# Kernel tuning notes

Measured on AMD Instinct MI355X. Metric: run time of the kernel, lower is better.

## Reference

```python
import jax, jax.numpy as jnp
import numpy as np

N_NODES = 100000
N_EDGES = 1600000
N_GRAPHS = 4096
IN_DIM = 14
HID = 128


def setup_inputs() -> dict:
    key = jax.random.key(0)
    ks = jax.random.split(key, 12)
    x = jax.random.normal(ks[0], (N_NODES, IN_DIM), dtype=jnp.float32)
    edge_index = jax.random.randint(ks[1], (2, N_EDGES), 0, N_NODES, dtype=jnp.int64)
    batch = jnp.sort(jax.random.randint(ks[2], (N_NODES,), 0, N_GRAPHS, dtype=jnp.int64))

    def lin(k, fan_in, fan_out):
        bound = 1.0 / np.sqrt(fan_in)
        kw, kb = jax.random.split(k)
        W = jax.random.uniform(kw, (fan_in, fan_out), minval=-bound, maxval=bound, dtype=jnp.float32)
        b = jax.random.uniform(kb, (fan_out,), minval=-bound, maxval=bound, dtype=jnp.float32)
        return W, b

    W1a, b1a = lin(ks[3], IN_DIM, HID)
    W1b, b1b = lin(ks[4], HID, HID)
    W2a, b2a = lin(ks[5], HID, HID)
    W2b, b2b = lin(ks[6], HID, HID)
    Wout, bout = lin(ks[7], HID, HID)
    return dict(x=x, edge_index=edge_index, batch=batch,
                W1a=W1a, b1a=b1a, W1b=W1b, b1b=b1b,
                W2a=W2a, b2a=b2a, W2b=W2b, b2b=b2b,
                Wout=Wout, bout=bout)


def _gin_conv(x, src, dst, Wa, ba, Wb, bb):
    # aggregate: sum of neighbor features x[src] scattered to dst; eps = 0
    agg = jax.ops.segment_sum(x[src], dst, num_segments=N_NODES)
    h = x + agg  # (1 + eps) * x + sum_j x_j, eps=0
    h = jax.nn.relu(h @ Wa + ba)
    return h @ Wb + bb


def reference(x, edge_index, batch, W1a, b1a, W1b, b1b, W2a, b2a, W2b, b2b, Wout, bout):
    src, dst = edge_index[0], edge_index[1]
    h = jax.nn.relu(_gin_conv(x, src, dst, W1a, b1a, W1b, b1b))
    h = jax.nn.relu(_gin_conv(h, src, dst, W2a, b2a, W2b, b2b))
    # global mean pool over graphs
    sums = jax.ops.segment_sum(h, batch, num_segments=N_GRAPHS)          # [G, HID]
    cnts = jax.ops.segment_sum(jnp.ones((h.shape[0],), h.dtype), batch, num_segments=N_GRAPHS)
    pooled = sums / jnp.maximum(cnts, 1.0)[:, None]
    # dropout is identity in eval mode
    return pooled @ Wout + bout
```

## Files before the change

### kernel.cpp

```cpp
#include <hip/hip_runtime.h>
#include <hip/hip_bf16.h>

#define NODES  100000
#define EDGES  1600000
#define GRAPHS 4096
#define HID    128
#define INDIM  14
#define NPART  8
#define PART_SZ ((NODES + NPART - 1) / NPART)
#define BPG    256
#define CSTRIDE 64
#define LDST   136

typedef float f32x4 __attribute__((ext_vector_type(4)));
typedef short bf16x8 __attribute__((ext_vector_type(8)));

__device__ __forceinline__ unsigned packbf(float a, float b) {
    __hip_bfloat162 t;
    t.x = __float2bfloat16(a);
    t.y = __float2bfloat16(b);
    return *(unsigned*)&t;
}
__device__ __forceinline__ void acc8(float* a, uint4 v) {
    a[0] += __uint_as_float(v.x << 16);
    a[1] += __uint_as_float(v.x & 0xffff0000u);
    a[2] += __uint_as_float(v.y << 16);
    a[3] += __uint_as_float(v.y & 0xffff0000u);
    a[4] += __uint_as_float(v.z << 16);
    a[5] += __uint_as_float(v.z & 0xffff0000u);
    a[6] += __uint_as_float(v.w << 16);
    a[7] += __uint_as_float(v.w & 0xffff0000u);
}


__global__ void k_zero_int(int* __restrict__ p, int n) {
    int i = blockIdx.x * 256 + threadIdx.x;
    if (i < n) p[i] = 0;
}

__global__ __launch_bounds__(256) void k_fill_fx(const int* __restrict__ src,
                                                 const int* __restrict__ dst,
                                                 int* __restrict__ cnt,
                                                 int* __restrict__ csr) {
    const int g = blockIdx.x & (NPART - 1);
    const int blk = blockIdx.x >> 3;
    const int lo = g * PART_SZ;
    for (int e = blk * 256 + threadIdx.x; e < EDGES; e += BPG * 256) {
        int d = __builtin_nontemporal_load(&dst[e]);
        if ((unsigned)(d - lo) < PART_SZ) {
            int s = __builtin_nontemporal_load(&src[e]);
            int pos = atomicAdd(&cnt[d], 1);
            if (pos < CSTRIDE) csr[d * CSTRIDE + pos] = s;
        }
    }
}


__global__ void k_w_cvt4(const float* __restrict__ Wa, const float* __restrict__ Wb,
                         const float* __restrict__ Wc, const float* __restrict__ Wd,
                         __hip_bfloat16* __restrict__ Ta, __hip_bfloat16* __restrict__ Tb,
                         __hip_bfloat16* __restrict__ Tc, __hip_bfloat16* __restrict__ Td) {
    int which = blockIdx.x >> 6;
    int idx = (blockIdx.x & 63) * 256 + threadIdx.x;
    const float* W = which == 0 ? Wa : which == 1 ? Wb : which == 2 ? Wc : Wd;
    __hip_bfloat16* T = which == 0 ? Ta : which == 1 ? Tb : which == 2 ? Tc : Td;
    int n = idx & 127, k = idx >> 7;
    T[n * HID + k] = __float2bfloat16(W[k * HID + n]);
}

template <int RELU, int TO_LDS>
__device__ __forceinline__ void mfma_slice16(const __hip_bfloat16* lds_in,
                                             const __hip_bfloat16* __restrict__ Wt,
                                             const float* __restrict__ bias,
                                             __hip_bfloat16* lds_out,
                                             __hip_bfloat16* __restrict__ gout,
                                             int row0, int tid) {
    const int wave = tid >> 6;
    const int lane = tid & 63;
    const int rl = lane & 15;
    const int kb = lane >> 4;

    bf16x8 afrag[4];
#pragma unroll
    for (int kc = 0; kc < 4; kc++)
        afrag[kc] = *(const bf16x8*)(lds_in + rl * LDST + kc * 32 + kb * 8);

#pragma unroll
    for (int s = 0; s < 2; s++) {
        const int n = wave * 2 + s;
        f32x4 acc = (f32x4){0.f, 0.f, 0.f, 0.f};
        const __hip_bfloat16* Bp = Wt + (size_t)(n * 16 + rl) * HID + kb * 8;
#pragma unroll
        for (int kc = 0; kc < 4; kc++) {
            bf16x8 bfrag = *(const bf16x8*)(Bp + kc * 32);
            acc = __builtin_amdgcn_mfma_f32_16x16x32_bf16(afrag[kc], bfrag, acc, 0, 0, 0);
        }
        const int col = n * 16 + rl;
        const float bv = bias[col];
#pragma unroll
        for (int j = 0; j < 4; j++) {
            int rloc = kb * 4 + j;
            float v = acc[j] + bv;
            if (RELU) v = fmaxf(v, 0.f);
            if (TO_LDS)
                lds_out[rloc * LDST + col] = __float2bfloat16(v);
            else
                gout[(size_t)(row0 + rloc) * HID + col] = __float2bfloat16(v);
        }
    }
}


__global__ __launch_bounds__(256) void k_l1(const float* __restrict__ x,
                                            const int* __restrict__ cnt,
                                            const int* __restrict__ csr,
                                            const float* __restrict__ W1a,
                                            const float* __restrict__ b1a,
                                            const __hip_bfloat16* __restrict__ Wt1b,
                                            const float* __restrict__ b1b,
                                            __hip_bfloat16* __restrict__ h1) {
    __shared__ float p14[16][16];
    __shared__ __hip_bfloat16 t[16 * LDST];
    const int row0 = blockIdx.x * 16;
    const int tid = threadIdx.x;

    {
        int n = tid >> 4, d = tid & 15;
        int node = row0 + n;
        if (d < INDIM) {
            int len = cnt[node];
            if (len > CSTRIDE) len = CSTRIDE;
            const int* cp = csr + (size_t)node * CSTRIDE;
            float acc = x[node * INDIM + d];
            int e = 0;
            for (; e + 3 < len; e += 4) {
                int s0 = cp[e], s1 = cp[e + 1], s2 = cp[e + 2], s3 = cp[e + 3];
                acc += x[s0 * INDIM + d] + x[s1 * INDIM + d] +
                       x[s2 * INDIM + d] + x[s3 * INDIM + d];
            }
            for (; e < len; e++) acc += x[cp[e] * INDIM + d];
            p14[n][d] = acc;
        }
    }
    __syncthreads();

    for (int i = tid; i < 512; i += 256) {
        int r = i >> 5, c4 = (i & 31) << 2;
        float4 bv = *(const float4*)&b1a[c4];
        float ax = bv.x, ay = bv.y, az = bv.z, aw = bv.w;
#pragma unroll
        for (int k = 0; k < INDIM; k++) {
            float a = p14[r][k];
            float4 w = *(const float4*)&W1a[k * HID + c4];
            ax += a * w.x; ay += a * w.y; az += a * w.z; aw += a * w.w;
        }
        unsigned p0 = packbf(fmaxf(ax, 0.f), fmaxf(ay, 0.f));
        unsigned p1 = packbf(fmaxf(az, 0.f), fmaxf(aw, 0.f));
        *(uint2*)&t[r * LDST + c4] = make_uint2(p0, p1);
    }
    __syncthreads();

    mfma_slice16<1, 0>(t, Wt1b, b1b, nullptr, h1, row0, tid);
}


__global__ __launch_bounds__(256) void k_l2(const uint4* __restrict__ H,
                                            const int* __restrict__ cnt,
                                            const int* __restrict__ csr,
                                            const __hip_bfloat16* __restrict__ Wt2a,
                                            const float* __restrict__ b2a,
                                            const __hip_bfloat16* __restrict__ Wt2b,
                                            const float* __restrict__ b2b,
                                            __hip_bfloat16* __restrict__ h2) {
    __shared__ __hip_bfloat16 ta[16 * LDST];
    __shared__ __hip_bfloat16 tb[16 * LDST];
    const int row0 = blockIdx.x * 16;
    const int tid = threadIdx.x;

    {
        int n = tid >> 4, q = tid & 15;
        int node = row0 + n;
        int len = cnt[node];
        if (len > CSTRIDE) len = CSTRIDE;
        const int* cp = csr + (size_t)node * CSTRIDE;
        float a[8];
        uint4 v = H[(size_t)node * 16 + q];
        a[0] = __uint_as_float(v.x << 16);
        a[1] = __uint_as_float(v.x & 0xffff0000u);
        a[2] = __uint_as_float(v.y << 16);
        a[3] = __uint_as_float(v.y & 0xffff0000u);
        a[4] = __uint_as_float(v.z << 16);
        a[5] = __uint_as_float(v.z & 0xffff0000u);
        a[6] = __uint_as_float(v.w << 16);
        a[7] = __uint_as_float(v.w & 0xffff0000u);
        int e = 0;
        for (; e + 3 < len; e += 4) {
            int s0 = cp[e], s1 = cp[e + 1], s2 = cp[e + 2], s3 = cp[e + 3];
            uint4 v0 = H[(size_t)s0 * 16 + q];
            uint4 v1 = H[(size_t)s1 * 16 + q];
            uint4 v2 = H[(size_t)s2 * 16 + q];
            uint4 v3 = H[(size_t)s3 * 16 + q];
            acc8(a, v0); acc8(a, v1); acc8(a, v2); acc8(a, v3);
        }
        for (; e < len; e++) {
            uint4 vv = H[(size_t)cp[e] * 16 + q];
            acc8(a, vv);
        }
        uint4 o;
        o.x = packbf(a[0], a[1]);
        o.y = packbf(a[2], a[3]);
        o.z = packbf(a[4], a[5]);
        o.w = packbf(a[6], a[7]);
        *(uint4*)&ta[n * LDST + q * 8] = o;
    }
    __syncthreads();

    mfma_slice16<1, 1>(ta, Wt2a, b2a, tb, nullptr, row0, tid);
    __syncthreads();

    mfma_slice16<1, 0>(tb, Wt2b, b2b, nullptr, h2, row0, tid);
}


__global__ __launch_bounds__(256) void k_head(const __hip_bfloat16* __restrict__ A,
                                              const __hip_bfloat16* __restrict__ Wt,
                                              const float* __restrict__ bias,
                                              float* __restrict__ out) {
    const int wave = threadIdx.x >> 6;
    const int lane = threadIdx.x & 63;
    const int row0 = blockIdx.x * 64 + wave * 16;
    const int rl = lane & 15;
    const int kb = lane >> 4;

    const __hip_bfloat16* Ap = A + (size_t)(row0 + rl) * HID + kb * 8;
    bf16x8 afrag[4];
#pragma unroll
    for (int kc = 0; kc < 4; kc++) afrag[kc] = *(const bf16x8*)(Ap + kc * 32);

#pragma unroll
    for (int n = 0; n < 8; n++) {
        f32x4 acc = (f32x4){0.f, 0.f, 0.f, 0.f};
        const __hip_bfloat16* Bp = Wt + (size_t)(n * 16 + rl) * HID + kb * 8;
#pragma unroll
        for (int kc = 0; kc < 4; kc++) {
            bf16x8 bfrag = *(const bf16x8*)(Bp + kc * 32);
            acc = __builtin_amdgcn_mfma_f32_16x16x32_bf16(afrag[kc], bfrag, acc, 0, 0, 0);
        }
        const int col = n * 16 + rl;
        const float bv = bias[col];
#pragma unroll
        for (int j = 0; j < 4; j++)
            out[(size_t)(row0 + kb * 4 + j) * HID + col] = acc[j] + bv;
    }
}


__device__ __forceinline__ int lower_bound_i(const int* __restrict__ a, int n, int key) {
    int lo = 0, hi = n;
    while (lo < hi) {
        int mid = (lo + hi) >> 1;
        if (a[mid] < key) lo = mid + 1; else hi = mid;
    }
    return lo;
}

__global__ __launch_bounds__(128) void k_pool(const __hip_bfloat16* __restrict__ H,
                                              const int* __restrict__ batch,
                                              __hip_bfloat16* __restrict__ pooled) {
    int g = blockIdx.x;
    int d = threadIdx.x;
    int lo = lower_bound_i(batch, NODES, g);
    int hi = lower_bound_i(batch, NODES, g + 1);
    float acc = 0.f;
    for (int i = lo; i < hi; i++) acc += __bfloat162float(H[(size_t)i * HID + d]);
    float cnt = (float)(hi - lo);
    pooled[(size_t)g * HID + d] = __float2bfloat16(acc / fmaxf(cnt, 1.0f));
}


extern "C" void kernel_launch(void* const* d_in, const int* in_sizes, int n_in,
                              void* d_out, int out_size, void* d_ws, size_t ws_size,
                              hipStream_t stream) {
    const float* x     = (const float*)d_in[0];
    const int*   ei    = (const int*)d_in[1];
    const int*   batch = (const int*)d_in[2];
    const float* W1a = (const float*)d_in[3];
    const float* b1a = (const float*)d_in[4];
    const float* W1b = (const float*)d_in[5];
    const float* b1b = (const float*)d_in[6];
    const float* W2a = (const float*)d_in[7];
    const float* b2a = (const float*)d_in[8];
    const float* W2b = (const float*)d_in[9];
    const float* b2b = (const float*)d_in[10];
    const float* Wout = (const float*)d_in[11];
    const float* bout = (const float*)d_in[12];

    const int* src = ei;
    const int* dst = ei + EDGES;

    char* w = (char*)d_ws;
    auto alloc = [&](size_t bytes) {
        void* p = (void*)w;
        w += (bytes + 255) & ~(size_t)255;
        return p;
    };
    __hip_bfloat16* h1 = (__hip_bfloat16*)alloc((size_t)NODES * HID * 2);
    __hip_bfloat16* h2 = (__hip_bfloat16*)alloc((size_t)NODES * HID * 2);
    __hip_bfloat16* pooled = (__hip_bfloat16*)alloc((size_t)GRAPHS * HID * 2);
    __hip_bfloat16* Wt1b = (__hip_bfloat16*)alloc(HID * HID * 2);
    __hip_bfloat16* Wt2a = (__hip_bfloat16*)alloc(HID * HID * 2);
    __hip_bfloat16* Wt2b = (__hip_bfloat16*)alloc(HID * HID * 2);
    __hip_bfloat16* Wtout = (__hip_bfloat16*)alloc(HID * HID * 2);
    int* cnt = (int*)alloc((size_t)NODES * 4);
    int* csr = (int*)alloc((size_t)NODES * CSTRIDE * 4);
    float* out = (float*)d_out;

    k_w_cvt4<<<256, 256, 0, stream>>>(W1b, W2a, W2b, Wout, Wt1b, Wt2a, Wt2b, Wtout);

    k_zero_int<<<(NODES + 255) / 256, 256, 0, stream>>>(cnt, NODES);
    k_fill_fx<<<NPART * BPG, 256, 0, stream>>>(src, dst, cnt, csr);

    k_l1<<<NODES / 16, 256, 0, stream>>>(x, cnt, csr, W1a, b1a, Wt1b, b1b, h1);
    k_l2<<<NODES / 16, 256, 0, stream>>>((const uint4*)h1, cnt, csr, Wt2a, b2a, Wt2b, b2b, h2);

    k_pool<<<GRAPHS, 128, 0, stream>>>(h2, batch, pooled);
    k_head<<<GRAPHS / 64, 256, 0, stream>>>(pooled, Wtout, bout, out);
}
```

Baseline: 275.4 us.

## Bucket edges by destination partition before CSR fill; store x as padded bf16

Replaces the CSR fill, where each of eight partition groups rescanned the whole edge list, with a two-pass scheme. One kernel reads the edges once and scatters (src,dst) pairs into per-partition buckets using block-local histograms. A second kernel then fills the CSR from each bucket with per-node atomics. It also fuses weight conversion, counter zeroing, and a new x-to-bf16 conversion padded to 16 columns into one prep kernel, so layer 1 gathers narrower, aligned rows. The cost is extra bucket memory traffic, a fixed bucket capacity that could overflow, and bf16 rounding of the input features.

```diff
diff --git a/kernel.cpp b/kernel.cpp
--- a/kernel.cpp
+++ b/kernel.cpp
@@ -8,12 +8,13 @@
 #define INDIM  14
 #define NPART  8
 #define PART_SZ ((NODES + NPART - 1) / NPART)
-#define BPG    256
 #define CSTRIDE 64
 #define LDST   136
+#define BUCKET_CAP 210000
 
 typedef float f32x4 __attribute__((ext_vector_type(4)));
 typedef short bf16x8 __attribute__((ext_vector_type(8)));
+typedef int   i32x4 __attribute__((ext_vector_type(4)));
 
 __device__ __forceinline__ unsigned packbf(float a, float b) {
     __hip_bfloat162 t;
@@ -33,40 +34,92 @@
 }
 
 
-__global__ void k_zero_int(int* __restrict__ p, int n) {
-    int i = blockIdx.x * 256 + threadIdx.x;
-    if (i < n) p[i] = 0;
-}
-
-__global__ __launch_bounds__(256) void k_fill_fx(const int* __restrict__ src,
-                                                 const int* __restrict__ dst,
-                                                 int* __restrict__ cnt,
-                                                 int* __restrict__ csr) {
-    const int g = blockIdx.x & (NPART - 1);
+__global__ void k_prep(const float* __restrict__ W1b, const float* __restrict__ W2a,
+                       const float* __restrict__ W2b, const float* __restrict__ Wout,
+                       __hip_bfloat16* __restrict__ T1b, __hip_bfloat16* __restrict__ T2a,
+                       __hip_bfloat16* __restrict__ T2b, __hip_bfloat16* __restrict__ Tout,
+                       const float* __restrict__ x, __hip_bfloat16* __restrict__ xb,
+                       int* __restrict__ cnt) {
+    int b = blockIdx.x;
+    if (b < 256) {
+        int which = b >> 6;
+        int idx = (b & 63) * 256 + threadIdx.x;
+        const float* W = which == 0 ? W1b : which == 1 ? W2a : which == 2 ? W2b : Wout;
+        __hip_bfloat16* T = which == 0 ? T1b : which == 1 ? T2a : which == 2 ? T2b : Tout;
+        int n = idx & 127, k = idx >> 7;
+        T[n * HID + k] = __float2bfloat16(W[k * HID + n]);
+    } else if (b < 256 + 6250) {
+        int idx = (b - 256) * 256 + threadIdx.x;
+        int node = idx >> 4, c = idx & 15;
+        xb[idx] = __float2bfloat16(c < INDIM ? x[node * INDIM + c] : 0.f);
+    } else {
+        int i = (b - 6506) * 256 + threadIdx.x;
+        if (i < NODES + NPART) cnt[i] = 0;
+    }
+}
+
+
+__global__ __launch_bounds__(256) void k_bucket(const i32x4* __restrict__ src4,
+                                                const i32x4* __restrict__ dst4,
+                                                int* __restrict__ bcnt,
+                                                uint2* __restrict__ bucket) {
+    __shared__ int lhist[NPART];
+    __shared__ int gbase[NPART];
+    const int tid = threadIdx.x;
+    const int n4 = EDGES / 4;
+    const int total = gridDim.x * 256;
+    const int iters = (n4 + total - 1) / total;
+    int idx = blockIdx.x * 256 + tid;
+    for (int it = 0; it < iters; it++, idx += total) {
+        bool act = idx < n4;
+        i32x4 d = (i32x4){0, 0, 0, 0}, s = (i32x4){0, 0, 0, 0};
+        if (act) {
+            d = __builtin_nontemporal_load(&dst4[idx]);
+            s = __builtin_nontemporal_load(&src4[idx]);
+        }
+        if (tid < NPART) lhist[tid] = 0;
+        __syncthreads();
+        int part[4], loff[4];
+#pragma unroll
+        for (int j = 0; j < 4; j++) {
+            part[j] = act ? (d[j] / PART_SZ) : -1;
+            loff[j] = (part[j] >= 0) ? atomicAdd(&lhist[part[j]], 1) : 0;
+        }
+        __syncthreads();
+        if (tid < NPART) gbase[tid] = atomicAdd(&bcnt[tid], lhist[tid]);
+        __syncthreads();
+#pragma unroll
+        for (int j = 0; j < 4; j++) {
+            if (part[j] >= 0) {
+                int pos = gbase[part[j]] + loff[j];
+                if (pos < BUCKET_CAP)
+                    bucket[(size_t)part[j] * BUCKET_CAP + pos] =
+                        make_uint2((unsigned)s[j], (unsigned)d[j]);
+            }
+        }
+        __syncthreads();
+    }
+}
+
+
+__global__ __launch_bounds__(256) void k_fill_b(const uint2* __restrict__ bucket,
+                                                const int* __restrict__ bcnt,
+                                                int* __restrict__ cnt,
+                                                int* __restrict__ csr) {
+    const int p = blockIdx.x & 7;
     const int blk = blockIdx.x >> 3;
-    const int lo = g * PART_SZ;
-    for (int e = blk * 256 + threadIdx.x; e < EDGES; e += BPG * 256) {
-        int d = __builtin_nontemporal_load(&dst[e]);
-        if ((unsigned)(d - lo) < PART_SZ) {
-            int s = __builtin_nontemporal_load(&src[e]);
-            int pos = atomicAdd(&cnt[d], 1);
-            if (pos < CSTRIDE) csr[d * CSTRIDE + pos] = s;
-        }
-    }
-}
-
-
-__global__ void k_w_cvt4(const float* __restrict__ Wa, const float* __restrict__ Wb,
-                         const float* __restrict__ Wc, const float* __restrict__ Wd,
-                         __hip_bfloat16* __restrict__ Ta, __hip_bfloat16* __restrict__ Tb,
-                         __hip_bfloat16* __restrict__ Tc, __hip_bfloat16* __restrict__ Td) {
-    int which = blockIdx.x >> 6;
-    int idx = (blockIdx.x & 63) * 256 + threadIdx.x;
-    const float* W = which == 0 ? Wa : which == 1 ? Wb : which == 2 ? Wc : Wd;
-    __hip_bfloat16* T = which == 0 ? Ta : which == 1 ? Tb : which == 2 ? Tc : Td;
-    int n = idx & 127, k = idx >> 7;
-    T[n * HID + k] = __float2bfloat16(W[k * HID + n]);
-}
+    int n = bcnt[p];
+    if (n > BUCKET_CAP) n = BUCKET_CAP;
+    const uint2* b = bucket + (size_t)p * BUCKET_CAP;
+    const int stride = (gridDim.x >> 3) * 256;
+    for (int i = blk * 256 + threadIdx.x; i < n; i += stride) {
+        uint2 pr = b[i];
+        int dj = (int)pr.y;
+        int pos = atomicAdd(&cnt[dj], 1);
+        if (pos < CSTRIDE) csr[dj * CSTRIDE + pos] = (int)pr.x;
+    }
+}
+
 
 template <int RELU, int TO_LDS>
 __device__ __forceinline__ void mfma_slice16(const __hip_bfloat16* lds_in,
@@ -111,7 +164,7 @@
 }
 
 
-__global__ __launch_bounds__(256) void k_l1(const float* __restrict__ x,
+__global__ __launch_bounds__(256) void k_l1(const __hip_bfloat16* __restrict__ xb,
                                             const int* __restrict__ cnt,
                                             const int* __restrict__ csr,
                                             const float* __restrict__ W1a,
@@ -131,14 +184,17 @@
             int len = cnt[node];
             if (len > CSTRIDE) len = CSTRIDE;
             const int* cp = csr + (size_t)node * CSTRIDE;
-            float acc = x[node * INDIM + d];
+            float acc = __bfloat162float(xb[node * 16 + d]);
             int e = 0;
             for (; e + 3 < len; e += 4) {
                 int s0 = cp[e], s1 = cp[e + 1], s2 = cp[e + 2], s3 = cp[e + 3];
-                acc += x[s0 * INDIM + d] + x[s1 * INDIM + d] +
-                       x[s2 * INDIM + d] + x[s3 * INDIM + d];
+                float v0 = __bfloat162float(xb[s0 * 16 + d]);
+                float v1 = __bfloat162float(xb[s1 * 16 + d]);
+                float v2 = __bfloat162float(xb[s2 * 16 + d]);
+                float v3 = __bfloat162float(xb[s3 * 16 + d]);
+                acc += (v0 + v1) + (v2 + v3);
             }
-            for (; e < len; e++) acc += x[cp[e] * INDIM + d];
+            for (; e < len; e++) acc += __bfloat162float(xb[cp[e] * 16 + d]);
             p14[n][d] = acc;
         }
     }
@@ -222,39 +278,6 @@
 }
 
 
-__global__ __launch_bounds__(256) void k_head(const __hip_bfloat16* __restrict__ A,
-                                              const __hip_bfloat16* __restrict__ Wt,
-                                              const float* __restrict__ bias,
-                                              float* __restrict__ out) {
-    const int wave = threadIdx.x >> 6;
-    const int lane = threadIdx.x & 63;
-    const int row0 = blockIdx.x * 64 + wave * 16;
-    const int rl = lane & 15;
-    const int kb = lane >> 4;
-
-    const __hip_bfloat16* Ap = A + (size_t)(row0 + rl) * HID + kb * 8;
-    bf16x8 afrag[4];
-#pragma unroll
-    for (int kc = 0; kc < 4; kc++) afrag[kc] = *(const bf16x8*)(Ap + kc * 32);
-
-#pragma unroll
-    for (int n = 0; n < 8; n++) {
-        f32x4 acc = (f32x4){0.f, 0.f, 0.f, 0.f};
-        const __hip_bfloat16* Bp = Wt + (size_t)(n * 16 + rl) * HID + kb * 8;
-#pragma unroll
-        for (int kc = 0; kc < 4; kc++) {
-            bf16x8 bfrag = *(const bf16x8*)(Bp + kc * 32);
-            acc = __builtin_amdgcn_mfma_f32_16x16x32_bf16(afrag[kc], bfrag, acc, 0, 0, 0);
-        }
-        const int col = n * 16 + rl;
-        const float bv = bias[col];
-#pragma unroll
-        for (int j = 0; j < 4; j++)
-            out[(size_t)(row0 + kb * 4 + j) * HID + col] = acc[j] + bv;
-    }
-}
-
-
 __device__ __forceinline__ int lower_bound_i(const int* __restrict__ a, int n, int key) {
     int lo = 0, hi = n;
     while (lo < hi) {
@@ -275,6 +298,39 @@
     for (int i = lo; i < hi; i++) acc += __bfloat162float(H[(size_t)i * HID + d]);
     float cnt = (float)(hi - lo);
     pooled[(size_t)g * HID + d] = __float2bfloat16(acc / fmaxf(cnt, 1.0f));
+}
+
+
+__global__ __launch_bounds__(256) void k_head(const __hip_bfloat16* __restrict__ A,
+                                              const __hip_bfloat16* __restrict__ Wt,
+                                              const float* __restrict__ bias,
+                                              float* __restrict__ out) {
+    const int wave = threadIdx.x >> 6;
+    const int lane = threadIdx.x & 63;
+    const int row0 = blockIdx.x * 64 + wave * 16;
+    const int rl = lane & 15;
+    const int kb = lane >> 4;
+
+    const __hip_bfloat16* Ap = A + (size_t)(row0 + rl) * HID + kb * 8;
+    bf16x8 afrag[4];
+#pragma unroll
+    for (int kc = 0; kc < 4; kc++) afrag[kc] = *(const bf16x8*)(Ap + kc * 32);
+
+#pragma unroll
+    for (int n = 0; n < 8; n++) {
+        f32x4 acc = (f32x4){0.f, 0.f, 0.f, 0.f};
+        const __hip_bfloat16* Bp = Wt + (size_t)(n * 16 + rl) * HID + kb * 8;
+#pragma unroll
+        for (int kc = 0; kc < 4; kc++) {
+            bf16x8 bfrag = *(const bf16x8*)(Bp + kc * 32);
+            acc = __builtin_amdgcn_mfma_f32_16x16x32_bf16(afrag[kc], bfrag, acc, 0, 0, 0);
+        }
+        const int col = n * 16 + rl;
+        const float bv = bias[col];
+#pragma unroll
+        for (int j = 0; j < 4; j++)
+            out[(size_t)(row0 + kb * 4 + j) * HID + col] = acc[j] + bv;
+    }
 }
 
 
@@ -304,6 +360,7 @@
         w += (bytes + 255) & ~(size_t)255;
         return p;
     };
+    __hip_bfloat16* xb = (__hip_bfloat16*)alloc((size_t)NODES * 16 * 2);
     __hip_bfloat16* h1 = (__hip_bfloat16*)alloc((size_t)NODES * HID * 2);
     __hip_bfloat16* h2 = (__hip_bfloat16*)alloc((size_t)NODES * HID * 2);
     __hip_bfloat16* pooled = (__hip_bfloat16*)alloc((size_t)GRAPHS * HID * 2);
@@ -311,16 +368,18 @@
     __hip_bfloat16* Wt2a = (__hip_bfloat16*)alloc(HID * HID * 2);
     __hip_bfloat16* Wt2b = (__hip_bfloat16*)alloc(HID * HID * 2);
     __hip_bfloat16* Wtout = (__hip_bfloat16*)alloc(HID * HID * 2);
-    int* cnt = (int*)alloc((size_t)NODES * 4);
+    int* cnt = (int*)alloc((size_t)(NODES + NPART) * 4);
+    int* bcnt = cnt + NODES;
     int* csr = (int*)alloc((size_t)NODES * CSTRIDE * 4);
+    uint2* bucket = (uint2*)alloc((size_t)NPART * BUCKET_CAP * 8);
     float* out = (float*)d_out;
 
-    k_w_cvt4<<<256, 256, 0, stream>>>(W1b, W2a, W2b, Wout, Wt1b, Wt2a, Wt2b, Wtout);
-
-    k_zero_int<<<(NODES + 255) / 256, 256, 0, stream>>>(cnt, NODES);
-    k_fill_fx<<<NPART * BPG, 256, 0, stream>>>(src, dst, cnt, csr);
-
-    k_l1<<<NODES / 16, 256, 0, stream>>>(x, cnt, csr, W1a, b1a, Wt1b, b1b, h1);
+    k_prep<<<6897, 256, 0, stream>>>(W1b, W2a, W2b, Wout, Wt1b, Wt2a, Wt2b, Wtout, x, xb, cnt);
+
+    k_bucket<<<384, 256, 0, stream>>>((const i32x4*)src, (const i32x4*)dst, bcnt, bucket);
+    k_fill_b<<<512, 256, 0, stream>>>(bucket, bcnt, cnt, csr);
+
+    k_l1<<<NODES / 16, 256, 0, stream>>>(xb, cnt, csr, W1a, b1a, Wt1b, b1b, h1);
     k_l2<<<NODES / 16, 256, 0, stream>>>((const uint4*)h1, cnt, csr, Wt2a, b2a, Wt2b, b2b, h2);
 
     k_pool<<<GRAPHS, 128, 0, stream>>>(h2, batch, pooled);
```

Measured after the change: 293.3 us. +6.5%, slower.
